# Optimization experiments

Hardware: AMD Instinct MI355X
Metric: run time of the kernel (lower is better)

Reference implementation:

```python
import jax, jax.numpy as jnp
import numpy as np

B, L, D, H, DFF, V, NL = 8, 512, 1024, 16, 4096, 32000, 6
DH = D // H
EPS = 1e-5


def _layer_norm(x):
    # fresh nn.LayerNorm(d_model) each call: gamma=1, beta=0
    mu = jnp.mean(x, axis=-1, keepdims=True)
    var = jnp.var(x, axis=-1, keepdims=True)
    return (x - mu) / jnp.sqrt(var + EPS)


def _positional_encoding(seq_len, d_model, dtype):
    position = jnp.arange(seq_len, dtype=jnp.float32)[:, None]
    div_term = 1.0 / jnp.power(10000.0, jnp.arange(0, d_model, 2, dtype=jnp.float32) / d_model)
    pe = jnp.zeros((seq_len, d_model), dtype=jnp.float32)
    pe = pe.at[:, 0::2].set(jnp.sin(position * div_term))
    pe = pe.at[:, 1::2].set(jnp.cos(position * div_term))
    return pe.astype(dtype)  # [L, D]


def setup_inputs() -> dict:
    key = jax.random.key(0)
    ks = jax.random.split(key, 16)
    s = 0.02
    inp = {
        "sequence": jax.random.randint(ks[0], (B, L), 0, V),
        "segment_label": jax.random.randint(ks[1], (B, L), 0, 3),
        "tok_emb": jax.random.normal(ks[2], (V, D), jnp.float32) * s,
        "seg_emb": jax.random.normal(ks[3], (3, D), jnp.float32) * s,
        "Wq": jax.random.normal(ks[4], (NL, D, D), jnp.float32) * s,
        "bq": jnp.zeros((NL, D), jnp.float32),
        "Wk": jax.random.normal(ks[5], (NL, D, D), jnp.float32) * s,
        "bk": jnp.zeros((NL, D), jnp.float32),
        "Wv": jax.random.normal(ks[6], (NL, D, D), jnp.float32) * s,
        "bv": jnp.zeros((NL, D), jnp.float32),
        "Wo": jax.random.normal(ks[7], (NL, D, D), jnp.float32) * s,
        "bo": jnp.zeros((NL, D), jnp.float32),
        "W1": jax.random.normal(ks[8], (NL, D, DFF), jnp.float32) * s,
        "b1": jnp.zeros((NL, DFF), jnp.float32),
        "W2": jax.random.normal(ks[9], (NL, DFF, D), jnp.float32) * s,
        "b2": jnp.zeros((NL, D), jnp.float32),
    }
    return inp


def reference(sequence, segment_label, tok_emb, seg_emb, Wq, bq, Wk, bk, Wv, bv, Wo, bo, W1, b1, W2, b2):
    n_layers = Wq.shape[0]
    batch, seq_len = sequence.shape
    d_model = tok_emb.shape[1]
    n_heads = H
    dh = d_model // n_heads

    # pad mask: True where key token == 0; broadcast over heads and query positions
    pad = (sequence == 0)  # [B, Lk]
    mask = pad[:, None, None, :]  # [B, 1, 1, Lk]

    pe = _positional_encoding(seq_len, d_model, tok_emb.dtype)
    x = tok_emb[sequence] + pe[None, :, :] + seg_emb[segment_label]  # [B, L, D]

    for i in range(n_layers):
        residual = x
        # NOTE: original code uses a raw reshape [B, L, H*dh] -> [B, H, L, dh]
        # (no transpose); we replicate that exact math.
        q = (x @ Wq[i] + bq[i]).reshape(batch, n_heads, seq_len, dh)
        k = (x @ Wk[i] + bk[i]).reshape(batch, n_heads, seq_len, dh)
        v = (x @ Wv[i] + bv[i]).reshape(batch, n_heads, seq_len, dh)
        scores = jnp.einsum("bhqd,bhkd->bhqk", q, k) / jnp.sqrt(jnp.asarray(dh, x.dtype))
        scores = jnp.where(mask, jnp.asarray(-1e9, x.dtype), scores)
        attn = jax.nn.softmax(scores, axis=-1)
        context = jnp.einsum("bhqk,bhkd->bhqd", attn, v).reshape(batch, seq_len, n_heads * dh)
        out = context @ Wo[i] + bo[i]
        x = _layer_norm(out + residual)

        residual = x
        h = jax.nn.gelu(x @ W1[i] + b1[i], approximate=False)
        out = h @ W2[i] + b2[i]
        x = _layer_norm(residual + out)

    return x
```

## Files before the change

### kernel.cpp

```cpp
#include <hip/hip_runtime.h>
#include <cstdint>
#include <cstddef>

typedef unsigned short u16;
typedef __attribute__((ext_vector_type(8))) short short8;
typedef __attribute__((ext_vector_type(4))) float f32x4;

#define DEV __device__ __forceinline__

DEV float bf2f(u16 u) {
    union { float f; uint32_t i; } c; c.i = ((uint32_t)u) << 16; return c.f;
}
DEV u16 f2bf(float f) {
    union { float f; uint32_t i; } c; c.f = f;
    uint32_t r = c.i + 0x7FFF + ((c.i >> 16) & 1);
    return (u16)(r >> 16);
}

DEV void gload16(const void* g, void* l) {
    __builtin_amdgcn_global_load_lds(
        (const __attribute__((address_space(1))) void*)g,
        (__attribute__((address_space(3))) void*)l, 16, 0, 0);
}

template<int N> DEV void waitv() {
    if constexpr (N == 0)      asm volatile("s_waitcnt vmcnt(0)" ::: "memory");
    else if constexpr (N == 2) asm volatile("s_waitcnt vmcnt(2)" ::: "memory");
    else if constexpr (N == 3) asm volatile("s_waitcnt vmcnt(3)" ::: "memory");
    else if constexpr (N == 4) asm volatile("s_waitcnt vmcnt(4)" ::: "memory");
    else if constexpr (N == 6) asm volatile("s_waitcnt vmcnt(6)" ::: "memory");
    else if constexpr (N == 8) asm volatile("s_waitcnt vmcnt(8)" ::: "memory");
    else                       asm volatile("s_waitcnt vmcnt(0)" ::: "memory");
}

template<int EPI>
__global__ __launch_bounds__(512)
void gemm256(const u16* __restrict__ A, const u16* __restrict__ B, void* __restrict__ C,
             const float* __restrict__ bias,
             int K, int lda, int ldb, int ldc)
{
    constexpr int THREADS = 512;
    constexpr int BM = 256, BN = 256, BK = 32;
    constexpr int MR = 8, NR = 4;
    __shared__ __align__(16) u16 As[3 * BM * BK];
    __shared__ __align__(16) u16 Bs[3 * BN * BK];

    const int tid = threadIdx.x, lane = tid & 63, wid = tid >> 6;
    const int wr = wid >> 2, wc = wid & 3;
    const int lr = lane & 15, lk = lane >> 4;
    const int m0 = blockIdx.x * BM, n0 = blockIdx.y * BN;

    f32x4 acc[MR][NR] = {};

    auto stageA = [&](int buf, int k0) {
#pragma unroll
        for (int i = 0; i < 2; ++i) {
            int ch = i * THREADS + tid;
            int rp = ch >> 3, s = ch & 7, d = s ^ (rp & 7);
            const u16* g = A + (long)(m0 + ((rp << 1) | (d & 1))) * lda + k0 + ((d >> 1) << 3);
            gload16(g, (char*)As + (size_t)buf * (BM * BK * 2) + ch * 16);
        }
    };
    auto stageB = [&](int buf, int k0) {
#pragma unroll
        for (int i = 0; i < 2; ++i) {
            int ch = i * THREADS + tid;
            int rp = ch >> 3, s = ch & 7, d = s ^ (rp & 7);
            const u16* g = B + (long)(n0 + ((rp << 1) | (d & 1))) * ldb + k0 + ((d >> 1) << 3);
            gload16(g, (char*)Bs + (size_t)buf * (BN * BK * 2) + ch * 16);
        }
    };
    auto lds_off = [&](int row) -> int {
        int rp = row >> 1;
        int s  = ((lk << 1) | (row & 1)) ^ (rp & 7);
        return rp * 64 + s * 8;
    };

    const int nt = K >> 5;

    stageA(0, 0); stageB(0, 0);
    if (nt > 1) { stageA(1, BK); stageB(1, BK); }
    if (nt > 1) waitv<4>(); else waitv<0>();
    __builtin_amdgcn_s_barrier();

    for (int k = 0; k < nt; ++k) {
        const int cur = k % 3;
        const int nxt = (k + 2) % 3;
        const u16* Ac = As + (size_t)cur * (BM * BK);
        const u16* Bc = Bs + (size_t)cur * (BN * BK);
        short8 af[MR], bf[NR];

#pragma unroll
        for (int n = 0; n < NR; ++n)
            bf[n] = *(const short8*)(Bc + lds_off(wc * 64 + n * 16 + lr));
#pragma unroll
        for (int m = 0; m < 4; ++m)
            af[m] = *(const short8*)(Ac + lds_off(wr * 128 + m * 16 + lr));
        if (k + 2 < nt) stageA(nxt, (k + 2) * BK);
        asm volatile("s_waitcnt lgkmcnt(0)" ::: "memory");
        __builtin_amdgcn_s_setprio(1);
#pragma unroll
        for (int m = 0; m < 4; ++m)
#pragma unroll
            for (int n = 0; n < NR; ++n)
                acc[m][n] = __builtin_amdgcn_mfma_f32_16x16x32_bf16(af[m], bf[n], acc[m][n], 0, 0, 0);
        __builtin_amdgcn_s_setprio(0);

#pragma unroll
        for (int m = 4; m < 8; ++m)
            af[m] = *(const short8*)(Ac + lds_off(wr * 128 + m * 16 + lr));
        if (k + 2 < nt) stageB(nxt, (k + 2) * BK);
        asm volatile("s_waitcnt lgkmcnt(0)" ::: "memory");
        __builtin_amdgcn_s_setprio(1);
#pragma unroll
        for (int m = 4; m < 8; ++m)
#pragma unroll
            for (int n = 0; n < NR; ++n)
                acc[m][n] = __builtin_amdgcn_mfma_f32_16x16x32_bf16(af[m], bf[n], acc[m][n], 0, 0, 0);
        __builtin_amdgcn_s_setprio(0);

        if (k + 1 < nt) {
            if (k + 2 < nt) waitv<4>(); else waitv<0>();
            __builtin_amdgcn_s_barrier();
        }
    }

#pragma unroll
    for (int m = 0; m < MR; ++m) {
        const int rowb = m0 + wr * 128 + m * 16 + (lane >> 4) * 4;
#pragma unroll
        for (int n = 0; n < NR; ++n) {
            const int col = n0 + wc * 64 + n * 16 + lr;
            const float bv = bias[col];
#pragma unroll
            for (int j = 0; j < 4; ++j) {
                float v = acc[m][n][j];
                if (EPI == 2) {
                    float t = v + bv;
                    ((u16*)C)[(long)(rowb + j) * ldc + col] =
                        f2bf(0.5f * t * (1.0f + erff(t * 0.70710678118654752f)));
                } else {
                    const long qidx = (long)(col >> 10) * 4194304L
                                    + (long)(rowb + j) * 1024 + (col & 1023);
                    ((u16*)C)[qidx] = f2bf(v + bv);
                }
            }
        }
    }
}

template<int WM, int WN, int MR, int NR, int EPI>
__global__ __launch_bounds__(WM * WN * 64)
void gemm_bt(const u16* __restrict__ A, const u16* __restrict__ B, void* __restrict__ C,
             const float* __restrict__ bias, const float* __restrict__ resid,
             int K, int lda, int ldb, int ldc,
             int nh, long a_zb, long a_zh, long b_zb, long b_zh, long c_zb, long c_zh,
             float scale)
{
    static_assert(WM * WN == 4 || WM * WN == 8, "4 or 8 waves");
    constexpr int THREADS = WM * WN * 64;
    constexpr int BM = WM * MR * 16;
    constexpr int BN = WN * NR * 16;
    constexpr int BK = 32;
    constexpr int NBUF = 3;
    __shared__ __align__(16) u16 As[NBUF * BM * BK];
    __shared__ __align__(16) u16 Bs[NBUF * BN * BK];

    const int tid  = threadIdx.x;
    const int lane = tid & 63;
    const int wid  = tid >> 6;
    const int zz = blockIdx.z;
    const int b = zz / nh, h = zz % nh;
    A += (long)b * a_zb + (long)h * a_zh;
    B += (long)b * b_zb + (long)h * b_zh;
    const long coff = (long)b * c_zb + (long)h * c_zh;
    const int m0 = blockIdx.x * BM, n0 = blockIdx.y * BN;

    f32x4 acc[MR][NR] = {};
    constexpr int AI = (BM * 4) / THREADS;
    constexpr int BI = (BN * 4) / THREADS;
    constexpr int L  = AI + BI;

    const int wr = wid / WN, wc = wid % WN;
    const int lr = lane & 15, lk = lane >> 4;

    auto stage = [&](int buf, int k0) {
#pragma unroll
        for (int i = 0; i < AI; ++i) {
            int ch = i * THREADS + tid;
            int rp = ch >> 3, s = ch & 7;
            int d  = s ^ (rp & 7);
            const u16* g = A + (long)(m0 + ((rp << 1) | (d & 1))) * lda + k0 + ((d >> 1) << 3);
            gload16(g, (char*)As + (size_t)buf * (BM * BK * 2) + ch * 16);
        }
#pragma unroll
        for (int i = 0; i < BI; ++i) {
            int ch = i * THREADS + tid;
            int rp = ch >> 3, s = ch & 7;
            int d  = s ^ (rp & 7);
            const u16* g = B + (long)(n0 + ((rp << 1) | (d & 1))) * ldb + k0 + ((d >> 1) << 3);
            gload16(g, (char*)Bs + (size_t)buf * (BN * BK * 2) + ch * 16);
        }
    };

    auto lds_off = [&](int row) -> int {
        int rp = row >> 1;
        int s  = ((lk << 1) | (row & 1)) ^ (rp & 7);
        return rp * 64 + s * 8;
    };

    const int nt = K >> 5;

    if (nt > 0) stage(0, 0);
    if (nt > 1) stage(1, BK);
    if (nt > 2) stage(2, 2 * BK);
    if (nt > 2)      waitv<2 * L>();
    else if (nt > 1) waitv<L>();
    else             waitv<0>();
    __builtin_amdgcn_s_barrier();

    for (int k = 0; k < nt; ++k) {
        const int cur = k % 3;
        const u16* Ac = As + (size_t)cur * (BM * BK);
        const u16* Bc = Bs + (size_t)cur * (BN * BK);
        short8 af[MR], bf[NR];
#pragma unroll
        for (int m = 0; m < MR; ++m)
            af[m] = *(const short8*)(Ac + lds_off(wr * MR * 16 + m * 16 + lr));
#pragma unroll
        for (int n = 0; n < NR; ++n)
            bf[n] = *(const short8*)(Bc + lds_off(wc * NR * 16 + n * 16 + lr));

        asm volatile("s_waitcnt lgkmcnt(0)" ::: "memory");
        __builtin_amdgcn_s_barrier();

        if (k + 3 < nt) stage(cur, (k + 3) * BK);

#pragma unroll
        for (int m = 0; m < MR; ++m)
#pragma unroll
            for (int n = 0; n < NR; ++n)
                acc[m][n] = __builtin_amdgcn_mfma_f32_16x16x32_bf16(af[m], bf[n], acc[m][n], 0, 0, 0);

        if (k + 1 < nt) {
            if (k + 4 <= nt)      waitv<2 * L>();
            else if (k + 3 == nt) waitv<L>();
            else                  waitv<0>();
            __builtin_amdgcn_s_barrier();
        }
    }

#pragma unroll
    for (int m = 0; m < MR; ++m) {
        const int rowb = m0 + wr * MR * 16 + m * 16 + (lane >> 4) * 4;
#pragma unroll
        for (int n = 0; n < NR; ++n) {
            const int col = n0 + wc * NR * 16 + n * 16 + lr;
            float bv = 0.f;
            if (EPI == 0 || EPI == 1 || EPI == 2 || EPI == 5) bv = bias[col];
#pragma unroll
            for (int j = 0; j < 4; ++j) {
                const long idx = coff + (long)(rowb + j) * ldc + col;
                float v = acc[m][n][j];
                if (EPI == 0) {
                    ((u16*)C)[idx] = f2bf(v + bv);
                } else if (EPI == 1) {
                    ((float*)C)[idx] = v + bv + resid[(long)(rowb + j) * ldc + col];
                } else if (EPI == 2) {
                    float t = v + bv;
                    ((u16*)C)[idx] = f2bf(0.5f * t * (1.0f + erff(t * 0.70710678118654752f)));
                } else if (EPI == 3) {
                    ((u16*)C)[idx] = f2bf(v * scale);
                } else if (EPI == 5) {
                    const long qidx = (long)(col >> 10) * 4194304L
                                    + (long)(rowb + j) * 1024 + (col & 1023);
                    ((u16*)C)[qidx] = f2bf(v + bv);
                } else {
                    ((u16*)C)[idx] = f2bf(v);
                }
            }
        }
    }
}

__global__ __launch_bounds__(256)
void wconv_kernel(const float* __restrict__ src, u16* __restrict__ dst,
                  int K, int N, int row_off)
{
    __shared__ __align__(16) float t[64][65];
    const float* s = src + (long)(blockIdx.y * 64) * N + blockIdx.x * 64;
    const int tid = threadIdx.x;
#pragma unroll
    for (int i = 0; i < 4; ++i) {
        int ch = (i << 8) + tid;
        int r = ch >> 4, c4 = ch & 15;
        float4 v = *(const float4*)(s + (long)r * N + c4 * 4);
        t[r][c4 * 4 + 0] = v.x; t[r][c4 * 4 + 1] = v.y;
        t[r][c4 * 4 + 2] = v.z; t[r][c4 * 4 + 3] = v.w;
    }
    __syncthreads();
    u16* d = dst + (long)(row_off + blockIdx.x * 64) * K + blockIdx.y * 64;
#pragma unroll
    for (int i = 0; i < 4; ++i) {
        int ch = (i << 8) + tid;
        int c = ch >> 4, k4 = ch & 15;
        ushort4 o;
        o.x = f2bf(t[k4 * 4 + 0][c]);
        o.y = f2bf(t[k4 * 4 + 1][c]);
        o.z = f2bf(t[k4 * 4 + 2][c]);
        o.w = f2bf(t[k4 * 4 + 3][c]);
        *(ushort4*)(d + (long)c * K + k4 * 4) = o;
    }
}

__global__ __launch_bounds__(256)
void bconcat_kernel(const float* __restrict__ bq, const float* __restrict__ bk,
                    const float* __restrict__ bv, float* __restrict__ out)
{
    int i = blockIdx.x * 256 + threadIdx.x;
    int l = i / 3072, n = i % 3072;
    float v = (n < 1024) ? bq[l * 1024 + n]
            : (n < 2048) ? bk[l * 1024 + n - 1024]
                         : bv[l * 1024 + n - 2048];
    out[i] = v;
}

__global__ __launch_bounds__(256)
void embed_kernel(const int* __restrict__ seq, const int* __restrict__ seg,
                  const float* __restrict__ tok, const float* __restrict__ sege,
                  float* __restrict__ x, u16* __restrict__ xb)
{
    long i = ((long)blockIdx.x << 8) + threadIdx.x;
    int d2 = (int)(i & 511);
    long bl = i >> 9;
    int l = (int)(bl & 511);
    int t = seq[bl];
    int g = seg[bl];
    float div = powf(10000.f, -(float)(2 * d2) * (1.0f / 1024.f));
    float arg = (float)l * div;
    float sv = sinf(arg), cv = cosf(arg);
    long toff = (long)t * 1024 + 2 * d2;
    long goff = (long)g * 1024 + 2 * d2;
    float x0 = tok[toff]     + sv + sege[goff];
    float x1 = tok[toff + 1] + cv + sege[goff + 1];
    long xo = (bl << 10) + 2 * d2;
    x[xo] = x0; x[xo + 1] = x1;
    xb[xo] = f2bf(x0); xb[xo + 1] = f2bf(x1);
}

__global__ __launch_bounds__(256)
void vtrans_kernel(const u16* __restrict__ Vb, u16* __restrict__ vt)
{
    __shared__ __align__(16) u16 t[64][72];
    const int bh = blockIdx.y;
    const int l0 = blockIdx.x << 6;
    const u16* src = Vb + ((long)bh << 15) + (long)l0 * 64;
    const int tid = threadIdx.x;
#pragma unroll
    for (int i = 0; i < 2; ++i) {
        int ch = (i << 8) + tid;
        int r = ch >> 3, c8 = ch & 7;
        short8 v = *(const short8*)(src + (long)r * 64 + (c8 << 3));
#pragma unroll
        for (int j = 0; j < 8; ++j) t[r][(c8 << 3) + j] = (u16)v[j];
    }
    __syncthreads();
    u16* d = vt + ((long)bh << 15) + l0;
#pragma unroll
    for (int i = 0; i < 2; ++i) {
        int ch = (i << 8) + tid;
        int dd = ch >> 3, l8 = ch & 7;
        short8 o;
#pragma unroll
        for (int j = 0; j < 8; ++j) o[j] = (short)t[(l8 << 3) + j][dd];
        *(short8*)(d + (long)dd * 512 + (l8 << 3)) = o;
    }
}

__global__ __launch_bounds__(256)
void softmax_kernel(u16* __restrict__ S, const int* __restrict__ seq)
{
    long row = ((long)blockIdx.x << 2) + (threadIdx.x >> 6);
    int lane = threadIdx.x & 63;
    int b = (int)(row >> 13);
    u16* p = S + (row << 9);
    short8 raw = *(short8*)(p + (lane << 3));
    const int* sq = seq + (b << 9) + (lane << 3);
    float v[8];
#pragma unroll
    for (int i = 0; i < 8; ++i)
        v[i] = (sq[i] == 0) ? -1e9f : bf2f((u16)raw[i]);
    float mx = v[0];
#pragma unroll
    for (int i = 1; i < 8; ++i) mx = fmaxf(mx, v[i]);
#pragma unroll
    for (int o = 32; o; o >>= 1) mx = fmaxf(mx, __shfl_xor(mx, o));
    float e[8], sum = 0.f;
#pragma unroll
    for (int i = 0; i < 8; ++i) { e[i] = expf(v[i] - mx); sum += e[i]; }
#pragma unroll
    for (int o = 32; o; o >>= 1) sum += __shfl_xor(sum, o);
    float r = 1.0f / sum;
    short8 o8;
#pragma unroll
    for (int i = 0; i < 8; ++i) o8[i] = (short)f2bf(e[i] * r);
    *(short8*)(p + (lane << 3)) = o8;
}

__global__ __launch_bounds__(256)
void ln_kernel(const float* __restrict__ in, float* __restrict__ xout, u16* __restrict__ xbout)
{
    const int row = blockIdx.x;
    const int tid = threadIdx.x;
    const float4 v = ((const float4*)(in + (long)row * 1024))[tid];
    float s = v.x + v.y + v.z + v.w;
#pragma unroll
    for (int o = 32; o; o >>= 1) s += __shfl_down(s, o);
    __shared__ float red[8];
    const int wid = tid >> 6, lane = tid & 63;
    if (lane == 0) red[wid] = s;
    __syncthreads();
    const float mean = (red[0] + red[1] + red[2] + red[3]) * (1.0f / 1024.f);
    const float dx = v.x - mean, dy = v.y - mean, dz = v.z - mean, dw = v.w - mean;
    float q = dx * dx + dy * dy + dz * dz + dw * dw;
#pragma unroll
    for (int o = 32; o; o >>= 1) q += __shfl_down(q, o);
    if (lane == 0) red[4 + wid] = q;
    __syncthreads();
    const float var = (red[4] + red[5] + red[6] + red[7]) * (1.0f / 1024.f);
    const float inv = rsqrtf(var + 1e-5f);
    float4 o4;
    o4.x = dx * inv; o4.y = dy * inv; o4.z = dz * inv; o4.w = dw * inv;
    ((float4*)(xout + (long)row * 1024))[tid] = o4;
    ushort4 ob;
    ob.x = f2bf(o4.x); ob.y = f2bf(o4.y); ob.z = f2bf(o4.z); ob.w = f2bf(o4.w);
    ((ushort4*)(xbout + (long)row * 1024))[tid] = ob;
}

extern "C" void kernel_launch(void* const* d_in, const int* in_sizes, int n_in,
                              void* d_out, int out_size, void* d_ws, size_t ws_size,
                              hipStream_t stream)
{
    const int*   seqp = (const int*)d_in[0];
    const int*   segp = (const int*)d_in[1];
    const float* tok  = (const float*)d_in[2];
    const float* sege = (const float*)d_in[3];
    const float* Wq = (const float*)d_in[4];  const float* bq = (const float*)d_in[5];
    const float* Wk = (const float*)d_in[6];  const float* bk = (const float*)d_in[7];
    const float* Wv = (const float*)d_in[8];  const float* bv = (const float*)d_in[9];
    const float* Wo = (const float*)d_in[10]; const float* bo = (const float*)d_in[11];
    const float* W1 = (const float*)d_in[12]; const float* b1 = (const float*)d_in[13];
    const float* W2 = (const float*)d_in[14]; const float* b2 = (const float*)d_in[15];

    char* w = (char*)d_ws;
    auto take = [&](size_t bytes) -> void* {
        void* p = (void*)w; w += (bytes + 255) & ~(size_t)255; return p;
    };
    float* x    = (float*)take(4096UL * 1024 * 4);
    u16*   xb   = (u16*)  take(4096UL * 1024 * 2);
    float* tmp  = (float*)take(4096UL * 1024 * 4);
    u16*   R1   = (u16*)  take(128UL * 512 * 512 * 2);
    u16*   qkv3 = (u16*)  take(3UL * 4096 * 1024 * 2);
    u16*   ctx  = (u16*)  take(4096UL * 1024 * 2);
    u16*   vt   = (u16*)  take(128UL * 64 * 512 * 2);
    u16*   qkvw = (u16*)  take(3072UL * 1024 * 2);
    u16*   wo_t = (u16*)  take(1024UL * 1024 * 2);
    u16*   w1_t = (u16*)  take(4096UL * 1024 * 2);
    u16*   w2_t = (u16*)  take(1024UL * 4096 * 2);
    float* bqkv = (float*)take(6UL * 3072 * 4);

    u16* S    = R1;
    u16* hbuf = R1;
    u16* Vb   = qkv3 + 8388608L;
    u16* Qb   = qkv3;
    u16* Kb   = qkv3 + 4194304L;

    bconcat_kernel<<<72, 256, 0, stream>>>(bq, bk, bv, bqkv);
    embed_kernel<<<8192, 256, 0, stream>>>(seqp, segp, tok, sege, x, xb);

    for (int l = 0; l < 6; ++l) {
        wconv_kernel<<<dim3(16, 16), 256, 0, stream>>>(Wq + (long)l * 1048576L, qkvw, 1024, 1024, 0);
        wconv_kernel<<<dim3(16, 16), 256, 0, stream>>>(Wk + (long)l * 1048576L, qkvw, 1024, 1024, 1024);
        wconv_kernel<<<dim3(16, 16), 256, 0, stream>>>(Wv + (long)l * 1048576L, qkvw, 1024, 1024, 2048);
        wconv_kernel<<<dim3(16, 16), 256, 0, stream>>>(Wo + (long)l * 1048576L, wo_t, 1024, 1024, 0);
        wconv_kernel<<<dim3(64, 16), 256, 0, stream>>>(W1 + (long)l * 4194304L, w1_t, 1024, 4096, 0);
        wconv_kernel<<<dim3(16, 64), 256, 0, stream>>>(W2 + (long)l * 4194304L, w2_t, 4096, 1024, 0);

        gemm256<5><<<dim3(16, 12), 512, 0, stream>>>(
            xb, qkvw, qkv3, bqkv + l * 3072, 1024, 1024, 1024, 1024);

        vtrans_kernel<<<dim3(8, 128), 256, 0, stream>>>(Vb, vt);

        gemm_bt<2, 2, 4, 4, 3><<<dim3(4, 4, 128), 256, 0, stream>>>(
            Qb, Kb, S, nullptr, nullptr,
            64, 64, 64, 512,
            16, 524288L, 32768L, 524288L, 32768L, 4194304L, 262144L, 0.125f);

        softmax_kernel<<<16384, 256, 0, stream>>>(S, seqp);

        gemm_bt<4, 1, 2, 4, 4><<<dim3(4, 1, 128), 256, 0, stream>>>(
            S, vt, ctx, nullptr, nullptr,
            512, 512, 512, 64,
            16, 4194304L, 262144L, 524288L, 32768L, 524288L, 32768L, 1.f);

        gemm_bt<2, 4, 4, 2, 1><<<dim3(32, 8, 1), 512, 0, stream>>>(
            ctx, wo_t, tmp, bo + l * 1024, x,
            1024, 1024, 1024, 1024, 1, 0, 0, 0, 0, 0, 0, 1.f);

        ln_kernel<<<4096, 256, 0, stream>>>(tmp, x, xb);

        gemm256<2><<<dim3(16, 16), 512, 0, stream>>>(
            xb, w1_t, hbuf, b1 + l * 4096, 1024, 1024, 1024, 4096);

        gemm_bt<2, 4, 4, 2, 1><<<dim3(32, 8, 1), 512, 0, stream>>>(
            hbuf, w2_t, tmp, b2 + l * 1024, x,
            4096, 4096, 4096, 1024, 1, 0, 0, 0, 0, 0, 0, 1.f);

        ln_kernel<<<4096, 256, 0, stream>>>(tmp, (l == 5) ? (float*)d_out : x, xb);
    }
}
```

Measured before the change: 1.779 ms.

## Fuse QK^T, masked softmax and PV into one attention kernel

Replaces the three-kernel attention path (scores GEMM, softmax, PV GEMM) with a single kernel in which each block handles 64 query rows of one head. The full 64x512 score tile is kept in XOR-swizzled shared memory, so the bf16 score matrix no longer goes to and from global memory and two launches are dropped. In exchange, Q, K and V fragments are read directly from global memory without LDS staging or pipelining. Occupancy is also limited by the 64 KB of shared memory per block.

```diff
diff --git a/kernel.cpp b/kernel.cpp
--- a/kernel.cpp
+++ b/kernel.cpp
@@ -31,6 +31,113 @@
     else if constexpr (N == 6) asm volatile("s_waitcnt vmcnt(6)" ::: "memory");
     else if constexpr (N == 8) asm volatile("s_waitcnt vmcnt(8)" ::: "memory");
     else                       asm volatile("s_waitcnt vmcnt(0)" ::: "memory");
+}
+
+__global__ __launch_bounds__(512)
+void attn_kernel(const u16* __restrict__ Qb, const u16* __restrict__ Kb,
+                 const u16* __restrict__ vt, const int* __restrict__ seq,
+                 u16* __restrict__ ctx)
+{
+    __shared__ __align__(16) u16 Ss[64 * 512];
+    const int tid = threadIdx.x, lane = tid & 63, wid = tid >> 6;
+    const int bh = blockIdx.y;
+    const int b  = bh >> 4;
+    const int q0 = blockIdx.x << 6;
+    const u16* Qh = Qb + ((long)bh << 15) + (long)q0 * 64;
+    const u16* Kh = Kb + ((long)bh << 15);
+    const u16* Vh = vt + ((long)bh << 15);
+    const int lr = lane & 15, lk = lane >> 4;
+
+    f32x4 sacc[4][4] = {};
+    {
+        short8 af[4], bf[4];
+#pragma unroll
+        for (int s = 0; s < 2; ++s) {
+#pragma unroll
+            for (int m = 0; m < 4; ++m)
+                af[m] = *(const short8*)(Qh + (long)(m * 16 + lr) * 64 + s * 32 + lk * 8);
+#pragma unroll
+            for (int n = 0; n < 4; ++n)
+                bf[n] = *(const short8*)(Kh + (long)(wid * 64 + n * 16 + lr) * 64 + s * 32 + lk * 8);
+#pragma unroll
+            for (int m = 0; m < 4; ++m)
+#pragma unroll
+                for (int n = 0; n < 4; ++n)
+                    sacc[m][n] = __builtin_amdgcn_mfma_f32_16x16x32_bf16(af[m], bf[n], sacc[m][n], 0, 0, 0);
+        }
+    }
+#pragma unroll
+    for (int m = 0; m < 4; ++m) {
+#pragma unroll
+        for (int n = 0; n < 4; ++n) {
+            const int k = wid * 64 + n * 16 + lr;
+#pragma unroll
+            for (int j = 0; j < 4; ++j) {
+                const int q = m * 16 + (lane >> 4) * 4 + j;
+                const int col = (((k >> 3) ^ (q & 7)) << 3) | (k & 7);
+                Ss[q * 512 + col] = f2bf(sacc[m][n][j] * 0.125f);
+            }
+        }
+    }
+    __syncthreads();
+
+    const int* sq = seq + (b << 9) + (lane << 3);
+    int msk[8];
+#pragma unroll
+    for (int i = 0; i < 8; ++i) msk[i] = sq[i];
+#pragma unroll
+    for (int r = 0; r < 8; ++r) {
+        const int q = wid * 8 + r;
+        u16* p = Ss + q * 512 + ((lane ^ (q & 7)) << 3);
+        short8 raw = *(short8*)p;
+        float v[8];
+#pragma unroll
+        for (int i = 0; i < 8; ++i)
+            v[i] = (msk[i] == 0) ? -1e9f : bf2f((u16)raw[i]);
+        float mx = v[0];
+#pragma unroll
+        for (int i = 1; i < 8; ++i) mx = fmaxf(mx, v[i]);
+#pragma unroll
+        for (int o = 32; o; o >>= 1) mx = fmaxf(mx, __shfl_xor(mx, o));
+        float e[8], sum = 0.f;
+#pragma unroll
+        for (int i = 0; i < 8; ++i) { e[i] = expf(v[i] - mx); sum += e[i]; }
+#pragma unroll
+        for (int o = 32; o; o >>= 1) sum += __shfl_xor(sum, o);
+        float rr = 1.0f / sum;
+        short8 o8;
+#pragma unroll
+        for (int i = 0; i < 8; ++i) o8[i] = (short)f2bf(e[i] * rr);
+        *(short8*)p = o8;
+    }
+    __syncthreads();
+
+    const int wr = wid >> 1, wc2 = wid & 1;
+    f32x4 pacc[2] = {};
+#pragma unroll
+    for (int ks = 0; ks < 16; ++ks) {
+        const int qrow = wr * 16 + lr;
+        short8 pa = *(const short8*)(Ss + qrow * 512 + (((ks * 4 + lk) ^ (qrow & 7)) << 3));
+        short8 vb[2];
+#pragma unroll
+        for (int n = 0; n < 2; ++n) {
+            const int d = wc2 * 32 + n * 16 + lr;
+            vb[n] = *(const short8*)(Vh + (long)d * 512 + ks * 32 + lk * 8);
+        }
+#pragma unroll
+        for (int n = 0; n < 2; ++n)
+            pacc[n] = __builtin_amdgcn_mfma_f32_16x16x32_bf16(pa, vb[n], pacc[n], 0, 0, 0);
+    }
+    u16* Ch = ctx + ((long)bh << 15) + (long)q0 * 64;
+#pragma unroll
+    for (int n = 0; n < 2; ++n) {
+        const int d = wc2 * 32 + n * 16 + lr;
+#pragma unroll
+        for (int j = 0; j < 4; ++j) {
+            const int q = wr * 16 + (lane >> 4) * 4 + j;
+            Ch[(long)q * 64 + d] = f2bf(pacc[n][j]);
+        }
+    }
 }
 
 template<int EPI>
@@ -378,36 +485,6 @@
 }
 
 __global__ __launch_bounds__(256)
-void softmax_kernel(u16* __restrict__ S, const int* __restrict__ seq)
-{
-    long row = ((long)blockIdx.x << 2) + (threadIdx.x >> 6);
-    int lane = threadIdx.x & 63;
-    int b = (int)(row >> 13);
-    u16* p = S + (row << 9);
-    short8 raw = *(short8*)(p + (lane << 3));
-    const int* sq = seq + (b << 9) + (lane << 3);
-    float v[8];
-#pragma unroll
-    for (int i = 0; i < 8; ++i)
-        v[i] = (sq[i] == 0) ? -1e9f : bf2f((u16)raw[i]);
-    float mx = v[0];
-#pragma unroll
-    for (int i = 1; i < 8; ++i) mx = fmaxf(mx, v[i]);
-#pragma unroll
-    for (int o = 32; o; o >>= 1) mx = fmaxf(mx, __shfl_xor(mx, o));
-    float e[8], sum = 0.f;
-#pragma unroll
-    for (int i = 0; i < 8; ++i) { e[i] = expf(v[i] - mx); sum += e[i]; }
-#pragma unroll
-    for (int o = 32; o; o >>= 1) sum += __shfl_xor(sum, o);
-    float r = 1.0f / sum;
-    short8 o8;
-#pragma unroll
-    for (int i = 0; i < 8; ++i) o8[i] = (short)f2bf(e[i] * r);
-    *(short8*)(p + (lane << 3)) = o8;
-}
-
-__global__ __launch_bounds__(256)
 void ln_kernel(const float* __restrict__ in, float* __restrict__ xout, u16* __restrict__ xbout)
 {
     const int row = blockIdx.x;
@@ -469,11 +546,10 @@
     u16*   w2_t = (u16*)  take(1024UL * 4096 * 2);
     float* bqkv = (float*)take(6UL * 3072 * 4);
 
-    u16* S    = R1;
     u16* hbuf = R1;
-    u16* Vb   = qkv3 + 8388608L;
     u16* Qb   = qkv3;
     u16* Kb   = qkv3 + 4194304L;
+    u16* Vb   = qkv3 + 8388608L;
 
     bconcat_kernel<<<72, 256, 0, stream>>>(bq, bk, bv, bqkv);
     embed_kernel<<<8192, 256, 0, stream>>>(seqp, segp, tok, sege, x, xb);
@@ -491,17 +567,7 @@
 
         vtrans_kernel<<<dim3(8, 128), 256, 0, stream>>>(Vb, vt);
 
-        gemm_bt<2, 2, 4, 4, 3><<<dim3(4, 4, 128), 256, 0, stream>>>(
-            Qb, Kb, S, nullptr, nullptr,
-            64, 64, 64, 512,
-            16, 524288L, 32768L, 524288L, 32768L, 4194304L, 262144L, 0.125f);
-
-        softmax_kernel<<<16384, 256, 0, stream>>>(S, seqp);
-
-        gemm_bt<4, 1, 2, 4, 4><<<dim3(4, 1, 128), 256, 0, stream>>>(
-            S, vt, ctx, nullptr, nullptr,
-            512, 512, 512, 64,
-            16, 4194304L, 262144L, 524288L, 32768L, 524288L, 32768L, 1.f);
+        attn_kernel<<<dim3(8, 128), 512, 0, stream>>>(Qb, Kb, vt, seqp, ctx);
 
         gemm_bt<2, 4, 4, 2, 1><<<dim3(32, 8, 1), 512, 0, stream>>>(
             ctx, wo_t, tmp, bo + l * 1024, x,
```

Result: faster. 1.744 ms (-2.0%).
